# Kernel tuning notes

Hardware: AMD Instinct MI355X
Metric: run time of the kernel (lower is better)

The kernel has to match this reference:

```python
import jax, jax.numpy as jnp
import numpy as np

B, C_IN, L = 8, 64, 4096
C_OUT, HEADS = 64, 3
E = 524288
T_DIM = 256
N = B * L
EPS = 1e-5
NEG_SLOPE = 0.2  # PyG GATConv default negative_slope


def setup_inputs() -> dict:
    key = jax.random.key(0)
    ks = jax.random.split(key, 12)
    x = jax.random.normal(ks[0], (B, C_IN, L), jnp.float32)
    time_emb = jax.random.normal(ks[1], (B, T_DIM), jnp.float32)
    edge_index = jax.random.randint(ks[2], (2, E), 0, N, dtype=jnp.int32)
    # GATConv params: lin maps in -> heads*out; att_src/att_dst per head
    W_lin = jax.random.normal(ks[3], (C_IN, HEADS * C_OUT), jnp.float32) / np.sqrt(C_IN)
    att_src = jax.random.normal(ks[4], (1, HEADS, C_OUT), jnp.float32) / np.sqrt(C_OUT)
    att_dst = jax.random.normal(ks[5], (1, HEADS, C_OUT), jnp.float32) / np.sqrt(C_OUT)
    bias = jnp.zeros((C_OUT,), jnp.float32)
    # time projection (computed but unused in the source forward)
    tp_W = jax.random.normal(ks[6], (T_DIM, C_OUT), jnp.float32) / np.sqrt(T_DIM)
    tp_b = jnp.zeros((C_OUT,), jnp.float32)
    # BatchNorm1d affine params (training-mode batch stats)
    gamma = jnp.ones((C_OUT,), jnp.float32)
    beta = jnp.zeros((C_OUT,), jnp.float32)
    return {"x": x, "time_emb": time_emb, "edge_index": edge_index,
            "W_lin": W_lin, "att_src": att_src, "att_dst": att_dst,
            "bias": bias, "tp_W": tp_W, "tp_b": tp_b,
            "gamma": gamma, "beta": beta}


def reference(x, time_emb, edge_index, W_lin, att_src, att_dst, bias, tp_W, tp_b, gamma, beta):
    b, c, l = x.shape
    n = b * l
    # time projection: present in source but its result is never used
    _t = (time_emb @ tp_W + tp_b)[:, :, None]  # [b, C_OUT, 1] (dead)
    h = (x.reshape(-1, c) @ W_lin).reshape(n, HEADS, C_OUT)  # [N,H,C]
    a_src = (h * att_src).sum(-1)  # [N,H]
    a_dst = (h * att_dst).sum(-1)  # [N,H]
    # add self loops (PyG default add_self_loops=True)
    loops = jnp.arange(n, dtype=edge_index.dtype)
    src = jnp.concatenate([edge_index[0], loops])
    dst = jnp.concatenate([edge_index[1], loops])
    e = a_src[src] + a_dst[dst]                        # [E+N, H]
    e = jnp.where(e > 0, e, NEG_SLOPE * e)             # LeakyReLU
    emax = jax.ops.segment_max(e, dst, num_segments=n)  # every node has a self loop
    ex = jnp.exp(e - emax[dst])
    denom = jax.ops.segment_sum(ex, dst, num_segments=n)
    alpha = ex / denom[dst]                            # segment softmax over dst
    msg = alpha[:, :, None] * h[src]                   # [E+N, H, C]
    out = jax.ops.segment_sum(msg, dst, num_segments=n)  # [N,H,C]
    out = out.mean(axis=1) + bias                      # concat=False -> head mean
    # BatchNorm1d (training mode: biased batch stats)
    mu = out.mean(axis=0)
    var = ((out - mu) ** 2).mean(axis=0)
    out = (out - mu) / jnp.sqrt(var + EPS) * gamma + beta
    out = jax.nn.relu(out)
    return out.reshape(b, -1, l)
```

## Files before the change

kernel.cpp:

```cpp
#include <hip/hip_runtime.h>
#include <hip/hip_bf16.h>

#define N_NODES 32768
#define E_EDGES 524288
#define HC 192
#define NEG_SLOPE 0.2f
#define BN_EPS 1e-5f
#define PAD 64

typedef _Float16 f16;
typedef __attribute__((ext_vector_type(8))) _Float16 v8h;
typedef __attribute__((ext_vector_type(4))) float    v4f;

#define GEMM_BLOCKS 512
#define SCAT_BLOCKS 512
#define FUSED_BLOCKS (GEMM_BLOCKS + SCAT_BLOCKS)

#define NODE_BLOCKS 8192
#define APPLY_BLOCKS 512

__device__ __forceinline__ float lrelu(float v) { return v > 0.f ? v : NEG_SLOPE * v; }

__device__ __forceinline__ float wave_sum(float v) {
#pragma unroll
    for (int off = 32; off > 0; off >>= 1) v += __shfl_xor(v, off);
    return v;
}
__device__ __forceinline__ float rlane(float v, int l) {
    return __uint_as_float(__builtin_amdgcn_readlane(__float_as_uint(v), l));
}

__global__ __launch_bounds__(256, 4) void k_fused(
        const int* __restrict__ esrc, const int* __restrict__ edst,
        int* __restrict__ cnt, unsigned short* __restrict__ csr_pad,
        const float* __restrict__ x, const float* __restrict__ W,
        const float* __restrict__ att_s, const float* __restrict__ att_d,
        f16* __restrict__ hh, float* __restrict__ a_src, float* __restrict__ a_dst,
        float* __restrict__ gp1, float* __restrict__ gp2) {
    const int bid = blockIdx.x;
    if (bid & 1) {
        const int base = (bid >> 1) * 1024 + threadIdx.x;
        int s0 = esrc[base];       int d0 = edst[base];
        int s1 = esrc[base + 256]; int d1 = edst[base + 256];
        int s2 = esrc[base + 512]; int d2 = edst[base + 512];
        int s3 = esrc[base + 768]; int d3 = edst[base + 768];
        int p0 = atomicAdd(&cnt[d0], 1);
        int p1 = atomicAdd(&cnt[d1], 1);
        int p2 = atomicAdd(&cnt[d2], 1);
        int p3 = atomicAdd(&cnt[d3], 1);
        if (p0 < PAD) csr_pad[d0 * PAD + p0] = (unsigned short)s0;
        if (p1 < PAD) csr_pad[d1 * PAD + p1] = (unsigned short)s1;
        if (p2 < PAD) csr_pad[d2 * PAD + p2] = (unsigned short)s2;
        if (p3 < PAD) csr_pad[d3 * PAD + p3] = (unsigned short)s3;
        return;
    }
    const int gid = bid >> 1;
    if (gid == 0) {
        float4 z = make_float4(0.f, 0.f, 0.f, 0.f);
#pragma unroll
        for (int i2 = 0; i2 < 4; i2++) {
            ((float4*)gp1)[threadIdx.x * 4 + i2] = z;
            ((float4*)gp2)[threadIdx.x * 4 + i2] = z;
        }
    }
    const int lane = threadIdx.x & 63;
    const int wid  = (gid * 256 + threadIdx.x) >> 6;
    const int q    = lane >> 4;
    const int nl   = lane & 15;
    const int n0   = wid * 16;

    v8h xf0, xf1;
    {
        const float* xr = x + (size_t)(n0 + nl) * 64 + q * 8;
        float4 lo = *(const float4*)(xr);
        float4 hi = *(const float4*)(xr + 4);
        xf0[0] = (f16)lo.x; xf0[1] = (f16)lo.y; xf0[2] = (f16)lo.z; xf0[3] = (f16)lo.w;
        xf0[4] = (f16)hi.x; xf0[5] = (f16)hi.y; xf0[6] = (f16)hi.z; xf0[7] = (f16)hi.w;
        lo = *(const float4*)(xr + 32);
        hi = *(const float4*)(xr + 36);
        xf1[0] = (f16)lo.x; xf1[1] = (f16)lo.y; xf1[2] = (f16)lo.z; xf1[3] = (f16)lo.w;
        xf1[4] = (f16)hi.x; xf1[5] = (f16)hi.y; xf1[6] = (f16)hi.z; xf1[7] = (f16)hi.w;
    }

    float sAcc = 0.f, dAcc = 0.f;
#pragma unroll
    for (int ct = 0; ct < 12; ct++) {
        const int c = ct * 16 + nl;
        v8h wf0, wf1;
#pragma unroll
        for (int j = 0; j < 8; j++) {
            wf0[j] = (f16)W[(q * 8 + j) * HC + c];
            wf1[j] = (f16)W[(32 + q * 8 + j) * HC + c];
        }
        float4 av = *(const float4*)(att_s + ct * 16 + q * 4);
        float4 dv = *(const float4*)(att_d + ct * 16 + q * 4);

        v4f C = {0.f, 0.f, 0.f, 0.f};
        C = __builtin_amdgcn_mfma_f32_16x16x32_f16(wf0, xf0, C, 0, 0, 0);
        C = __builtin_amdgcn_mfma_f32_16x16x32_f16(wf1, xf1, C, 0, 0, 0);

        union { f16 h[4]; unsigned long long u; } pk;
        pk.h[0] = (f16)C[0]; pk.h[1] = (f16)C[1];
        pk.h[2] = (f16)C[2]; pk.h[3] = (f16)C[3];
        *(unsigned long long*)(hh + (size_t)(n0 + nl) * HC + ct * 16 + q * 4) = pk.u;

        sAcc = fmaf(C[0], av.x, sAcc); sAcc = fmaf(C[1], av.y, sAcc);
        sAcc = fmaf(C[2], av.z, sAcc); sAcc = fmaf(C[3], av.w, sAcc);
        dAcc = fmaf(C[0], dv.x, dAcc); dAcc = fmaf(C[1], dv.y, dAcc);
        dAcc = fmaf(C[2], dv.z, dAcc); dAcc = fmaf(C[3], dv.w, dAcc);

        if ((ct & 3) == 3) {
            float s = sAcc; s += __shfl_xor(s, 16); s += __shfl_xor(s, 32);
            float d = dAcc; d += __shfl_xor(d, 16); d += __shfl_xor(d, 32);
            if (lane < 16) {
                a_src[(n0 + lane) * 4 + (ct >> 2)] = s;
                a_dst[(n0 + lane) * 4 + (ct >> 2)] = d;
            }
            sAcc = 0.f; dAcc = 0.f;
        }
    }
}

__global__ __launch_bounds__(256, 8) void k_node(
        const f16* __restrict__ hh,
        const float* __restrict__ a_src,
        const float* __restrict__ a_dst,
        const int* __restrict__ cnt,
        const unsigned short* __restrict__ csr_pad,
        const float* __restrict__ bias,
        float* __restrict__ out_pre,
        float* __restrict__ gp1,
        float* __restrict__ gp2) {
    const int lane = threadIdx.x & 63;
    const int wv = threadIdx.x >> 6;
    const int n = blockIdx.x * 4 + wv;

    int deg = cnt[n]; if (deg > PAD) deg = PAD;
    const unsigned short* __restrict__ row = csr_pad + n * PAD;

    const float ad0 = a_dst[n * 4 + 0], ad1 = a_dst[n * 4 + 1], ad2 = a_dst[n * 4 + 2];

    float ws0 = __expf(lrelu(a_src[n * 4 + 0] + ad0));
    float ws1 = __expf(lrelu(a_src[n * 4 + 1] + ad1));
    float ws2 = __expf(lrelu(a_src[n * 4 + 2] + ad2));
    float den0 = ws0, den1 = ws1, den2 = ws2;
    const f16* hn = hh + (size_t)n * HC;
    float acc0 = ws0 * (float)hn[lane];
    float acc1 = ws1 * (float)hn[64 + lane];
    float acc2 = ws2 * (float)hn[128 + lane];

    int s = 0;
    float w0 = 0.f, w1 = 0.f, w2 = 0.f;
    if (lane < deg) {
        s = (int)row[lane];
        float4 as = ((const float4*)a_src)[s];
        w0 = __expf(lrelu(as.x + ad0));
        w1 = __expf(lrelu(as.y + ad1));
        w2 = __expf(lrelu(as.z + ad2));
    }
    den0 += wave_sum(w0);
    den1 += wave_sum(w1);
    den2 += wave_sum(w2);

    int j = 0;
    for (; j + 8 <= deg; j += 8) {
#pragma unroll
        for (int u = 0; u < 8; u += 4) {
            int s0 = __builtin_amdgcn_readlane(s, j + u);
            int s1 = __builtin_amdgcn_readlane(s, j + u + 1);
            int s2 = __builtin_amdgcn_readlane(s, j + u + 2);
            int s3 = __builtin_amdgcn_readlane(s, j + u + 3);
            const f16* __restrict__ h0 = hh + (size_t)s0 * HC;
            const f16* __restrict__ h1 = hh + (size_t)s1 * HC;
            const f16* __restrict__ h2 = hh + (size_t)s2 * HC;
            const f16* __restrict__ h3 = hh + (size_t)s3 * HC;
            float v00 = (float)h0[lane], v01 = (float)h0[64 + lane], v02 = (float)h0[128 + lane];
            float v10 = (float)h1[lane], v11 = (float)h1[64 + lane], v12 = (float)h1[128 + lane];
            float v20 = (float)h2[lane], v21 = (float)h2[64 + lane], v22 = (float)h2[128 + lane];
            float v30 = (float)h3[lane], v31 = (float)h3[64 + lane], v32 = (float)h3[128 + lane];
            float w00 = rlane(w0, j + u),     w01 = rlane(w1, j + u),     w02 = rlane(w2, j + u);
            float w10 = rlane(w0, j + u + 1), w11 = rlane(w1, j + u + 1), w12 = rlane(w2, j + u + 1);
            float w20 = rlane(w0, j + u + 2), w21 = rlane(w1, j + u + 2), w22 = rlane(w2, j + u + 2);
            float w30 = rlane(w0, j + u + 3), w31 = rlane(w1, j + u + 3), w32 = rlane(w2, j + u + 3);
            acc0 = fmaf(w00, v00, acc0); acc0 = fmaf(w10, v10, acc0);
            acc0 = fmaf(w20, v20, acc0); acc0 = fmaf(w30, v30, acc0);
            acc1 = fmaf(w01, v01, acc1); acc1 = fmaf(w11, v11, acc1);
            acc1 = fmaf(w21, v21, acc1); acc1 = fmaf(w31, v31, acc1);
            acc2 = fmaf(w02, v02, acc2); acc2 = fmaf(w12, v12, acc2);
            acc2 = fmaf(w22, v22, acc2); acc2 = fmaf(w32, v32, acc2);
        }
    }
    for (; j < deg; j++) {
        int sa = __builtin_amdgcn_readlane(s, j);
        const f16* __restrict__ ha = hh + (size_t)sa * HC;
        float wa0 = rlane(w0, j), wa1 = rlane(w1, j), wa2 = rlane(w2, j);
        acc0 = fmaf(wa0, (float)ha[lane], acc0);
        acc1 = fmaf(wa1, (float)ha[64 + lane], acc1);
        acc2 = fmaf(wa2, (float)ha[128 + lane], acc2);
    }

    float outv = (acc0 / den0 + acc1 / den1 + acc2 / den2) * (1.0f / 3.0f) + bias[lane];
    out_pre[n * 64 + lane] = outv;

    __shared__ float ls[4][64], lq[4][64];
    ls[wv][lane] = outv;
    lq[wv][lane] = outv * outv;
    __syncthreads();
    if (threadIdx.x < 64) {
        int t = threadIdx.x;
        float s_ = ls[0][t] + ls[1][t] + ls[2][t] + ls[3][t];
        float q_ = lq[0][t] + lq[1][t] + lq[2][t] + lq[3][t];
        int slice = blockIdx.x & 63;
        atomicAdd(&gp1[slice * 64 + t], s_);
        atomicAdd(&gp2[slice * 64 + t], q_);
    }
}

__global__ __launch_bounds__(256) void k_apply(const float4* __restrict__ out_pre4,
                                               const float* __restrict__ gp1,
                                               const float* __restrict__ gp2,
                                               const float* __restrict__ gamma,
                                               const float* __restrict__ beta,
                                               float4* __restrict__ out4) {
    __shared__ float sc[64], sh[64];
    __shared__ float rs[256], rq[256];
    {
        const int t = threadIdx.x & 63, g = threadIdx.x >> 6;
        float s = 0.f, q = 0.f;
#pragma unroll
        for (int i = 0; i < 16; i++) {
            s += gp1[(g * 16 + i) * 64 + t];
            q += gp2[(g * 16 + i) * 64 + t];
        }
        rs[threadIdx.x] = s;
        rq[threadIdx.x] = q;
    }
    __syncthreads();
    if (threadIdx.x < 64) {
        int t = threadIdx.x;
        float s = rs[t] + rs[64 + t] + rs[128 + t] + rs[192 + t];
        float q = rq[t] + rq[64 + t] + rq[128 + t] + rq[192 + t];
        const float inv_n = 1.0f / (float)N_NODES;
        float mu = s * inv_n;
        float var = q * inv_n - mu * mu;
        float invstd = 1.0f / sqrtf(var + BN_EPS);
        float scale = invstd * gamma[t];
        sc[t] = scale;
        sh[t] = beta[t] - mu * scale;
    }
    __syncthreads();
    const int total = N_NODES * 64 / 4;
    for (int idx = blockIdx.x * 256 + threadIdx.x; idx < total; idx += APPLY_BLOCKS * 256) {
        int c0 = (idx * 4) & 63;
        float4 v = out_pre4[idx];
        float4 r;
        r.x = fmaxf(v.x * sc[c0 + 0] + sh[c0 + 0], 0.f);
        r.y = fmaxf(v.y * sc[c0 + 1] + sh[c0 + 1], 0.f);
        r.z = fmaxf(v.z * sc[c0 + 2] + sh[c0 + 2], 0.f);
        r.w = fmaxf(v.w * sc[c0 + 3] + sh[c0 + 3], 0.f);
        out4[idx] = r;
    }
}

extern "C" void kernel_launch(void* const* d_in, const int* in_sizes, int n_in,
                              void* d_out, int out_size, void* d_ws, size_t ws_size,
                              hipStream_t stream) {
    const float* x     = (const float*)d_in[0];
    const int*   ei    = (const int*)d_in[2];
    const float* W     = (const float*)d_in[3];
    const float* att_s = (const float*)d_in[4];
    const float* att_d = (const float*)d_in[5];
    const float* bias  = (const float*)d_in[6];
    const float* gamma = (const float*)d_in[9];
    const float* beta  = (const float*)d_in[10];
    float* out = (float*)d_out;

    char* ws = (char*)d_ws;
    size_t off = 0;
    auto alloc = [&](size_t bytes) -> void* {
        void* p = ws + off;
        off += (bytes + 255) & ~(size_t)255;
        return p;
    };
    f16*            hh      = (f16*)alloc((size_t)N_NODES * HC * 2);
    float*          a_src   = (float*)alloc((size_t)N_NODES * 4 * 4);
    float*          a_dst   = (float*)alloc((size_t)N_NODES * 4 * 4);
    int*            cnt     = (int*)alloc((size_t)N_NODES * 4);
    unsigned short* csr_pad = (unsigned short*)alloc((size_t)N_NODES * PAD * 2);
    float*          out_pre = (float*)alloc((size_t)N_NODES * 64 * 4);
    float*          gp1     = (float*)alloc(64 * 64 * 4);
    float*          gp2     = (float*)alloc(64 * 64 * 4);

    hipMemsetAsync(cnt, 0, (size_t)N_NODES * 4, stream);

    k_fused<<<FUSED_BLOCKS, 256, 0, stream>>>(
        ei, ei + E_EDGES, cnt, csr_pad,
        x, W, att_s, att_d, hh, a_src, a_dst, gp1, gp2);
    k_node<<<NODE_BLOCKS, 256, 0, stream>>>(hh, a_src, a_dst, cnt, csr_pad, bias,
                                            out_pre, gp1, gp2);
    k_apply<<<APPLY_BLOCKS, 256, 0, stream>>>((const float4*)out_pre, gp1, gp2,
                                              gamma, beta, (float4*)out);
}
```

Before: 143.2 us.

## Aggregate raw x before projection and fold attention vectors into W

Uses linearity to reorder the work. Attention scores are computed as x·(W·att), and the softmax-weighted aggregation gathers 64-wide fp16 x rows per head instead of 192-wide projected h rows. A new MFMA GEMM kernel then multiplies the aggregated per-head features by W (with the 1/3 head mean folded in), adds the bias and accumulates the BatchNorm partial sums. This shrinks the random-gather traffic in the edge loop, at the cost of an extra kernel launch, an intermediate Z buffer, and every block redundantly recomputing W·att.

```diff
diff --git a/kernel.cpp b/kernel.cpp
--- a/kernel.cpp
+++ b/kernel.cpp
@@ -1,5 +1,4 @@
 #include <hip/hip_runtime.h>
-#include <hip/hip_bf16.h>
 
 #define N_NODES 32768
 #define E_EDGES 524288
@@ -12,11 +11,11 @@
 typedef __attribute__((ext_vector_type(8))) _Float16 v8h;
 typedef __attribute__((ext_vector_type(4))) float    v4f;
 
+#define SCAT_BLOCKS 512
+#define ASCORE_BLOCKS 512
+#define FUSED_BLOCKS (SCAT_BLOCKS + ASCORE_BLOCKS)
+#define NODE_BLOCKS 8192
 #define GEMM_BLOCKS 512
-#define SCAT_BLOCKS 512
-#define FUSED_BLOCKS (GEMM_BLOCKS + SCAT_BLOCKS)
-
-#define NODE_BLOCKS 8192
 #define APPLY_BLOCKS 512
 
 __device__ __forceinline__ float lrelu(float v) { return v > 0.f ? v : NEG_SLOPE * v; }
@@ -25,9 +24,6 @@
 #pragma unroll
     for (int off = 32; off > 0; off >>= 1) v += __shfl_xor(v, off);
     return v;
-}
-__device__ __forceinline__ float rlane(float v, int l) {
-    return __uint_as_float(__builtin_amdgcn_readlane(__float_as_uint(v), l));
 }
 
 __global__ __launch_bounds__(256, 4) void k_fused(
@@ -35,11 +31,11 @@
         int* __restrict__ cnt, unsigned short* __restrict__ csr_pad,
         const float* __restrict__ x, const float* __restrict__ W,
         const float* __restrict__ att_s, const float* __restrict__ att_d,
-        f16* __restrict__ hh, float* __restrict__ a_src, float* __restrict__ a_dst,
-        float* __restrict__ gp1, float* __restrict__ gp2) {
+        f16* __restrict__ x16, float* __restrict__ a_src, float* __restrict__ a_dst,
+        f16* __restrict__ Wp, float* __restrict__ gp1, float* __restrict__ gp2) {
     const int bid = blockIdx.x;
-    if (bid & 1) {
-        const int base = (bid >> 1) * 1024 + threadIdx.x;
+    if (bid < SCAT_BLOCKS) {
+        const int base = bid * 1024 + threadIdx.x;
         int s0 = esrc[base];       int d0 = edst[base];
         int s1 = esrc[base + 256]; int d1 = edst[base + 256];
         int s2 = esrc[base + 512]; int d2 = edst[base + 512];
@@ -54,83 +50,67 @@
         if (p3 < PAD) csr_pad[d3 * PAD + p3] = (unsigned short)s3;
         return;
     }
-    const int gid = bid >> 1;
+    const int gid = bid - SCAT_BLOCKS;
+    __shared__ float us[3][64], ud[3][64];
+    if (threadIdx.x < 192) {
+        const int h = threadIdx.x >> 6, k = threadIdx.x & 63;
+        const float* wr = W + k * HC + h * 64;
+        const float* ap = att_s + h * 64;
+        const float* dp = att_d + h * 64;
+        float su = 0.f, du = 0.f;
+#pragma unroll
+        for (int ch = 0; ch < 64; ch++) {
+            float w = wr[ch];
+            su = fmaf(w, ap[ch], su);
+            du = fmaf(w, dp[ch], du);
+        }
+        us[h][k] = su; ud[h][k] = du;
+    }
     if (gid == 0) {
-        float4 z = make_float4(0.f, 0.f, 0.f, 0.f);
-#pragma unroll
-        for (int i2 = 0; i2 < 4; i2++) {
-            ((float4*)gp1)[threadIdx.x * 4 + i2] = z;
-            ((float4*)gp2)[threadIdx.x * 4 + i2] = z;
-        }
-    }
-    const int lane = threadIdx.x & 63;
-    const int wid  = (gid * 256 + threadIdx.x) >> 6;
-    const int q    = lane >> 4;
-    const int nl   = lane & 15;
-    const int n0   = wid * 16;
-
-    v8h xf0, xf1;
-    {
-        const float* xr = x + (size_t)(n0 + nl) * 64 + q * 8;
-        float4 lo = *(const float4*)(xr);
-        float4 hi = *(const float4*)(xr + 4);
-        xf0[0] = (f16)lo.x; xf0[1] = (f16)lo.y; xf0[2] = (f16)lo.z; xf0[3] = (f16)lo.w;
-        xf0[4] = (f16)hi.x; xf0[5] = (f16)hi.y; xf0[6] = (f16)hi.z; xf0[7] = (f16)hi.w;
-        lo = *(const float4*)(xr + 32);
-        hi = *(const float4*)(xr + 36);
-        xf1[0] = (f16)lo.x; xf1[1] = (f16)lo.y; xf1[2] = (f16)lo.z; xf1[3] = (f16)lo.w;
-        xf1[4] = (f16)hi.x; xf1[5] = (f16)hi.y; xf1[6] = (f16)hi.z; xf1[7] = (f16)hi.w;
-    }
-
-    float sAcc = 0.f, dAcc = 0.f;
-#pragma unroll
-    for (int ct = 0; ct < 12; ct++) {
-        const int c = ct * 16 + nl;
-        v8h wf0, wf1;
-#pragma unroll
-        for (int j = 0; j < 8; j++) {
-            wf0[j] = (f16)W[(q * 8 + j) * HC + c];
-            wf1[j] = (f16)W[(32 + q * 8 + j) * HC + c];
-        }
-        float4 av = *(const float4*)(att_s + ct * 16 + q * 4);
-        float4 dv = *(const float4*)(att_d + ct * 16 + q * 4);
-
-        v4f C = {0.f, 0.f, 0.f, 0.f};
-        C = __builtin_amdgcn_mfma_f32_16x16x32_f16(wf0, xf0, C, 0, 0, 0);
-        C = __builtin_amdgcn_mfma_f32_16x16x32_f16(wf1, xf1, C, 0, 0, 0);
-
-        union { f16 h[4]; unsigned long long u; } pk;
-        pk.h[0] = (f16)C[0]; pk.h[1] = (f16)C[1];
-        pk.h[2] = (f16)C[2]; pk.h[3] = (f16)C[3];
-        *(unsigned long long*)(hh + (size_t)(n0 + nl) * HC + ct * 16 + q * 4) = pk.u;
-
-        sAcc = fmaf(C[0], av.x, sAcc); sAcc = fmaf(C[1], av.y, sAcc);
-        sAcc = fmaf(C[2], av.z, sAcc); sAcc = fmaf(C[3], av.w, sAcc);
-        dAcc = fmaf(C[0], dv.x, dAcc); dAcc = fmaf(C[1], dv.y, dAcc);
-        dAcc = fmaf(C[2], dv.z, dAcc); dAcc = fmaf(C[3], dv.w, dAcc);
-
-        if ((ct & 3) == 3) {
-            float s = sAcc; s += __shfl_xor(s, 16); s += __shfl_xor(s, 32);
-            float d = dAcc; d += __shfl_xor(d, 16); d += __shfl_xor(d, 32);
-            if (lane < 16) {
-                a_src[(n0 + lane) * 4 + (ct >> 2)] = s;
-                a_dst[(n0 + lane) * 4 + (ct >> 2)] = d;
+        float4 z4 = make_float4(0.f, 0.f, 0.f, 0.f);
+#pragma unroll
+        for (int i = 0; i < 4; i++) {
+            ((float4*)gp1)[threadIdx.x * 4 + i] = z4;
+            ((float4*)gp2)[threadIdx.x * 4 + i] = z4;
+        }
+        for (int idx = threadIdx.x; idx < 1536; idx += 256) {
+            const int kfct = idx >> 6, ln = idx & 63;
+            const int kf = kfct >> 2, ct = kfct & 3;
+            const int qq = ln >> 4, nn = ln & 15;
+#pragma unroll
+            for (int j = 0; j < 8; j++) {
+                int kp = kf * 32 + qq * 8 + j;
+                int h = kp >> 6, kk = kp & 63;
+                Wp[(size_t)idx * 8 + j] = (f16)W[kk * HC + h * 64 + ct * 16 + nn];
             }
-            sAcc = 0.f; dAcc = 0.f;
+        }
+    }
+    __syncthreads();
+    const int lane = threadIdx.x & 63, wv = threadIdx.x >> 6;
+    const float u0 = us[0][lane], u1 = us[1][lane], u2 = us[2][lane];
+    const float d0 = ud[0][lane], d1 = ud[1][lane], d2 = ud[2][lane];
+    const int nbase = (gid * 4 + wv) * 16;
+#pragma unroll 1
+    for (int t = 0; t < 16; t++) {
+        const int n = nbase + t;
+        const float xv = x[n * 64 + lane];
+        x16[n * 64 + lane] = (f16)xv;
+        float s0 = wave_sum(xv * u0), s1 = wave_sum(xv * u1), s2 = wave_sum(xv * u2);
+        float t0 = wave_sum(xv * d0), t1 = wave_sum(xv * d1), t2 = wave_sum(xv * d2);
+        if (lane == 0) {
+            ((float4*)a_src)[n] = make_float4(s0, s1, s2, 0.f);
+            ((float4*)a_dst)[n] = make_float4(t0, t1, t2, 0.f);
         }
     }
 }
 
 __global__ __launch_bounds__(256, 8) void k_node(
-        const f16* __restrict__ hh,
+        const f16* __restrict__ x16,
         const float* __restrict__ a_src,
         const float* __restrict__ a_dst,
         const int* __restrict__ cnt,
         const unsigned short* __restrict__ csr_pad,
-        const float* __restrict__ bias,
-        float* __restrict__ out_pre,
-        float* __restrict__ gp1,
-        float* __restrict__ gp2) {
+        f16* __restrict__ Z) {
     const int lane = threadIdx.x & 63;
     const int wv = threadIdx.x >> 6;
     const int n = blockIdx.x * 4 + wv;
@@ -143,11 +123,6 @@
     float ws0 = __expf(lrelu(a_src[n * 4 + 0] + ad0));
     float ws1 = __expf(lrelu(a_src[n * 4 + 1] + ad1));
     float ws2 = __expf(lrelu(a_src[n * 4 + 2] + ad2));
-    float den0 = ws0, den1 = ws1, den2 = ws2;
-    const f16* hn = hh + (size_t)n * HC;
-    float acc0 = ws0 * (float)hn[lane];
-    float acc1 = ws1 * (float)hn[64 + lane];
-    float acc2 = ws2 * (float)hn[128 + lane];
 
     int s = 0;
     float w0 = 0.f, w1 = 0.f, w2 = 0.f;
@@ -158,58 +133,98 @@
         w1 = __expf(lrelu(as.y + ad1));
         w2 = __expf(lrelu(as.z + ad2));
     }
-    den0 += wave_sum(w0);
-    den1 += wave_sum(w1);
-    den2 += wave_sum(w2);
+    float den0 = ws0 + wave_sum(w0);
+    float den1 = ws1 + wave_sum(w1);
+    float den2 = ws2 + wave_sum(w2);
+    const float i0 = 1.f / (3.f * den0);
+    const float i1 = 1.f / (3.f * den1);
+    const float i2 = 1.f / (3.f * den2);
+
+    __shared__ float4 wsl[4][64];
+    wsl[wv][lane] = make_float4(w0 * i0, w1 * i1, w2 * i2, __int_as_float(s));
+
+    const float xs = (float)x16[n * 64 + lane];
+    float z0 = ws0 * i0 * xs, z1 = ws1 * i1 * xs, z2 = ws2 * i2 * xs;
 
     int j = 0;
     for (; j + 8 <= deg; j += 8) {
-#pragma unroll
-        for (int u = 0; u < 8; u += 4) {
-            int s0 = __builtin_amdgcn_readlane(s, j + u);
-            int s1 = __builtin_amdgcn_readlane(s, j + u + 1);
-            int s2 = __builtin_amdgcn_readlane(s, j + u + 2);
-            int s3 = __builtin_amdgcn_readlane(s, j + u + 3);
-            const f16* __restrict__ h0 = hh + (size_t)s0 * HC;
-            const f16* __restrict__ h1 = hh + (size_t)s1 * HC;
-            const f16* __restrict__ h2 = hh + (size_t)s2 * HC;
-            const f16* __restrict__ h3 = hh + (size_t)s3 * HC;
-            float v00 = (float)h0[lane], v01 = (float)h0[64 + lane], v02 = (float)h0[128 + lane];
-            float v10 = (float)h1[lane], v11 = (float)h1[64 + lane], v12 = (float)h1[128 + lane];
-            float v20 = (float)h2[lane], v21 = (float)h2[64 + lane], v22 = (float)h2[128 + lane];
-            float v30 = (float)h3[lane], v31 = (float)h3[64 + lane], v32 = (float)h3[128 + lane];
-            float w00 = rlane(w0, j + u),     w01 = rlane(w1, j + u),     w02 = rlane(w2, j + u);
-            float w10 = rlane(w0, j + u + 1), w11 = rlane(w1, j + u + 1), w12 = rlane(w2, j + u + 1);
-            float w20 = rlane(w0, j + u + 2), w21 = rlane(w1, j + u + 2), w22 = rlane(w2, j + u + 2);
-            float w30 = rlane(w0, j + u + 3), w31 = rlane(w1, j + u + 3), w32 = rlane(w2, j + u + 3);
-            acc0 = fmaf(w00, v00, acc0); acc0 = fmaf(w10, v10, acc0);
-            acc0 = fmaf(w20, v20, acc0); acc0 = fmaf(w30, v30, acc0);
-            acc1 = fmaf(w01, v01, acc1); acc1 = fmaf(w11, v11, acc1);
-            acc1 = fmaf(w21, v21, acc1); acc1 = fmaf(w31, v31, acc1);
-            acc2 = fmaf(w02, v02, acc2); acc2 = fmaf(w12, v12, acc2);
-            acc2 = fmaf(w22, v22, acc2); acc2 = fmaf(w32, v32, acc2);
+        int sj[8]; float xv[8];
+#pragma unroll
+        for (int u = 0; u < 8; u++) sj[u] = __builtin_amdgcn_readlane(s, j + u);
+#pragma unroll
+        for (int u = 0; u < 8; u++) xv[u] = (float)x16[(size_t)sj[u] * 64 + lane];
+#pragma unroll
+        for (int u = 0; u < 8; u++) {
+            float4 wj = wsl[wv][j + u];
+            z0 = fmaf(wj.x, xv[u], z0);
+            z1 = fmaf(wj.y, xv[u], z1);
+            z2 = fmaf(wj.z, xv[u], z2);
         }
     }
     for (; j < deg; j++) {
         int sa = __builtin_amdgcn_readlane(s, j);
-        const f16* __restrict__ ha = hh + (size_t)sa * HC;
-        float wa0 = rlane(w0, j), wa1 = rlane(w1, j), wa2 = rlane(w2, j);
-        acc0 = fmaf(wa0, (float)ha[lane], acc0);
-        acc1 = fmaf(wa1, (float)ha[64 + lane], acc1);
-        acc2 = fmaf(wa2, (float)ha[128 + lane], acc2);
-    }
-
-    float outv = (acc0 / den0 + acc1 / den1 + acc2 / den2) * (1.0f / 3.0f) + bias[lane];
-    out_pre[n * 64 + lane] = outv;
-
-    __shared__ float ls[4][64], lq[4][64];
-    ls[wv][lane] = outv;
-    lq[wv][lane] = outv * outv;
+        float xa = (float)x16[(size_t)sa * 64 + lane];
+        float4 wj = wsl[wv][j];
+        z0 = fmaf(wj.x, xa, z0);
+        z1 = fmaf(wj.y, xa, z1);
+        z2 = fmaf(wj.z, xa, z2);
+    }
+
+    f16* zr = Z + (size_t)n * HC;
+    zr[lane]       = (f16)z0;
+    zr[64 + lane]  = (f16)z1;
+    zr[128 + lane] = (f16)z2;
+}
+
+__global__ __launch_bounds__(256, 4) void k_gemm(
+        const f16* __restrict__ Z, const f16* __restrict__ Wp,
+        const float* __restrict__ bias,
+        float* __restrict__ out_pre,
+        float* __restrict__ gp1, float* __restrict__ gp2) {
+    const int lane = threadIdx.x & 63, wv = threadIdx.x >> 6;
+    const int q = lane >> 4, nl = lane & 15;
+    const int n0 = (blockIdx.x * 4 + wv) * 16;
+
+    v4f C[4] = {{0.f,0.f,0.f,0.f},{0.f,0.f,0.f,0.f},{0.f,0.f,0.f,0.f},{0.f,0.f,0.f,0.f}};
+#pragma unroll
+    for (int kf = 0; kf < 6; kf++) {
+        v8h zb = *(const v8h*)(Z + (size_t)(n0 + nl) * HC + kf * 32 + q * 8);
+#pragma unroll
+        for (int ct = 0; ct < 4; ct++) {
+            v8h wa = *(const v8h*)(Wp + ((size_t)(kf * 4 + ct) * 64 + lane) * 8);
+            C[ct] = __builtin_amdgcn_mfma_f32_16x16x32_f16(wa, zb, C[ct], 0, 0, 0);
+        }
+    }
+
+    __shared__ float bs[4][64], bq[4][64];
+#pragma unroll
+    for (int ct = 0; ct < 4; ct++) {
+        const int ch0 = ct * 16 + q * 4;
+        float4 bv = *(const float4*)(bias + ch0);
+        float o0 = C[ct][0] + bv.x, o1 = C[ct][1] + bv.y;
+        float o2 = C[ct][2] + bv.z, o3 = C[ct][3] + bv.w;
+        *(float4*)(out_pre + (size_t)(n0 + nl) * 64 + ch0) = make_float4(o0, o1, o2, o3);
+        float r0 = o0, r1 = o1, r2 = o2, r3 = o3;
+        float s0 = o0 * o0, s1 = o1 * o1, s2 = o2 * o2, s3 = o3 * o3;
+#pragma unroll
+        for (int off = 1; off < 16; off <<= 1) {
+            r0 += __shfl_xor(r0, off); r1 += __shfl_xor(r1, off);
+            r2 += __shfl_xor(r2, off); r3 += __shfl_xor(r3, off);
+            s0 += __shfl_xor(s0, off); s1 += __shfl_xor(s1, off);
+            s2 += __shfl_xor(s2, off); s3 += __shfl_xor(s3, off);
+        }
+        if (nl == 0) {
+            bs[wv][ch0 + 0] = r0; bs[wv][ch0 + 1] = r1;
+            bs[wv][ch0 + 2] = r2; bs[wv][ch0 + 3] = r3;
+            bq[wv][ch0 + 0] = s0; bq[wv][ch0 + 1] = s1;
+            bq[wv][ch0 + 2] = s2; bq[wv][ch0 + 3] = s3;
+        }
+    }
     __syncthreads();
     if (threadIdx.x < 64) {
         int t = threadIdx.x;
-        float s_ = ls[0][t] + ls[1][t] + ls[2][t] + ls[3][t];
-        float q_ = lq[0][t] + lq[1][t] + lq[2][t] + lq[3][t];
+        float s_ = bs[0][t] + bs[1][t] + bs[2][t] + bs[3][t];
+        float q_ = bq[0][t] + bq[1][t] + bq[2][t] + bq[3][t];
         int slice = blockIdx.x & 63;
         atomicAdd(&gp1[slice * 64 + t], s_);
         atomicAdd(&gp2[slice * 64 + t], q_);
@@ -282,11 +297,13 @@
         off += (bytes + 255) & ~(size_t)255;
         return p;
     };
-    f16*            hh      = (f16*)alloc((size_t)N_NODES * HC * 2);
+    f16*            x16     = (f16*)alloc((size_t)N_NODES * 64 * 2);
     float*          a_src   = (float*)alloc((size_t)N_NODES * 4 * 4);
     float*          a_dst   = (float*)alloc((size_t)N_NODES * 4 * 4);
     int*            cnt     = (int*)alloc((size_t)N_NODES * 4);
     unsigned short* csr_pad = (unsigned short*)alloc((size_t)N_NODES * PAD * 2);
+    f16*            Z       = (f16*)alloc((size_t)N_NODES * HC * 2);
+    f16*            Wp      = (f16*)alloc((size_t)1536 * 8 * 2);
     float*          out_pre = (float*)alloc((size_t)N_NODES * 64 * 4);
     float*          gp1     = (float*)alloc(64 * 64 * 4);
     float*          gp2     = (float*)alloc(64 * 64 * 4);
@@ -295,9 +312,9 @@
 
     k_fused<<<FUSED_BLOCKS, 256, 0, stream>>>(
         ei, ei + E_EDGES, cnt, csr_pad,
-        x, W, att_s, att_d, hh, a_src, a_dst, gp1, gp2);
-    k_node<<<NODE_BLOCKS, 256, 0, stream>>>(hh, a_src, a_dst, cnt, csr_pad, bias,
-                                            out_pre, gp1, gp2);
+        x, W, att_s, att_d, x16, a_src, a_dst, Wp, gp1, gp2);
+    k_node<<<NODE_BLOCKS, 256, 0, stream>>>(x16, a_src, a_dst, cnt, csr_pad, Z);
+    k_gemm<<<GEMM_BLOCKS, 256, 0, stream>>>(Z, Wp, bias, out_pre, gp1, gp2);
     k_apply<<<APPLY_BLOCKS, 256, 0, stream>>>((const float4*)out_pre, gp1, gp2,
                                               gamma, beta, (float4*)out);
 }
```

Result: slower. 163.7 us (+14.4%).
